# Kernel tuning notes

Measured on AMD Instinct MI355X. Metric: run time of the kernel, lower is better.

Reference implementation:

```python
import jax, jax.numpy as jnp
import numpy as np

B, S, N, F = 4, 256, 128, 64
D = 128          # d_model == 2*F so encoder/decoder dims agree
NH = 4           # hard-coded num_heads in both MHA blocks


def _linear(x, w, b):
    # torch nn.Linear: y = x @ W.T + b, W: (out, in)
    return x @ w.T + b


def _mha(q, k, v, w_in, b_in, w_out, b_out, nh):
    # torch nn.MultiheadAttention (batch_first=True) with packed in_proj
    bq, sq, e = q.shape
    hd = e // nh
    qp = _linear(q, w_in[:e], b_in[:e])
    kp = _linear(k, w_in[e:2 * e], b_in[e:2 * e])
    vp = _linear(v, w_in[2 * e:], b_in[2 * e:])
    qh = qp.reshape(bq, sq, nh, hd)
    kh = kp.reshape(bq, k.shape[1], nh, hd)
    vh = vp.reshape(bq, v.shape[1], nh, hd)
    scores = jnp.einsum('bqhd,bkhd->bhqk', qh, kh) / np.sqrt(hd).astype(np.float32)
    attn = jax.nn.softmax(scores, axis=-1)
    out = jnp.einsum('bhqk,bkhd->bqhd', attn, vh).reshape(bq, sq, e)
    return _linear(out, w_out, b_out)


def _pos_enc(s, d):
    pos = jnp.arange(s, dtype=jnp.float32)[:, None]
    div = jnp.exp(jnp.arange(0, d, 2, dtype=jnp.float32) * (-np.log(10000.0) / d))
    pe = jnp.zeros((s, d), dtype=jnp.float32)
    pe = pe.at[:, 0::2].set(jnp.sin(pos * div))
    pe = pe.at[:, 1::2].set(jnp.cos(pos * div))
    return pe


def _haar_decouple(x):
    # exact vectorized pywt haar dwt + single-branch idwt (even seq_len)
    b, s, n, f = x.shape
    pairs = x.reshape(b, s // 2, 2, n, f)
    avg = (pairs[:, :, 0] + pairs[:, :, 1]) * 0.5  # idwt(cA, None) value
    dif = (pairs[:, :, 0] - pairs[:, :, 1]) * 0.5  # idwt(None, cD) value
    x_l = jnp.stack([avg, avg], axis=2).reshape(b, s, n, f)
    x_h = jnp.stack([dif, -dif], axis=2).reshape(b, s, n, f)
    return x_l, x_h


def setup_inputs() -> dict:
    key = jax.random.key(0)
    ks = jax.random.split(key, 32)
    p = lambda i, shp: jax.random.normal(ks[i], shp, jnp.float32) * 0.02
    return {
        'x': jax.random.normal(ks[0], (B, S, N, F), jnp.float32),
        'ts': jax.random.randint(ks[1], (B, S), 0, 252),
        'ta_w_in': p(2, (3 * D, D)), 'ta_b_in': p(3, (3 * D,)),
        'ta_w_out': p(4, (D, D)), 'ta_b_out': p(5, (D,)),
        'conv_w': p(6, (D, 2 * F, 3)), 'conv_b': p(7, (D,)),
        'pl_w': p(8, (D, D)), 'pl_b': p(9, (D,)),
        'ph_w': p(10, (D, D)), 'ph_b': p(11, (D,)),
        'as_w_in': p(12, (3 * D, D)), 'as_b_in': p(13, (3 * D,)),
        'as_w_out': p(14, (D, D)), 'as_b_out': p(15, (D,)),
        'ac_w_in': p(16, (3 * D, D)), 'ac_b_in': p(17, (3 * D,)),
        'ac_w_out': p(18, (D, D)), 'ac_b_out': p(19, (D,)),
        'rl_w': p(20, (1, D)), 'rl_b': p(21, (1,)),
        'cl_w': p(22, (2, D)), 'cl_b': p(23, (2,)),
        'rf_w': p(24, (1, D)), 'rf_b': p(25, (1,)),
        'cf_w': p(26, (2, D)), 'cf_b': p(27, (2,)),
    }


def reference(x, ts, ta_w_in, ta_b_in, ta_w_out, ta_b_out, conv_w, conv_b,
              pl_w, pl_b, ph_w, ph_b, as_w_in, as_b_in, as_w_out, as_b_out,
              ac_w_in, ac_b_in, ac_w_out, ac_b_out, rl_w, rl_b, cl_w, cl_b,
              rf_w, rf_b, cf_w, cf_b):
    b, s, n, f = x.shape
    # --- DecouplingFlowLayer (vectorized haar) ---
    x_l, x_h = _haar_decouple(x)
    xl_cat = jnp.concatenate([x, x_l], axis=-1)  # (b,s,n,2f)
    xh_cat = jnp.concatenate([x, x_h], axis=-1)
    e = 2 * f
    # --- DualFrequencyEncoder ---
    pe = _pos_enc(s, e)
    xl_flat = xl_cat.transpose(0, 2, 1, 3).reshape(b * n, s, e) + pe
    x_tatt = _mha(xl_flat, xl_flat, xl_flat, ta_w_in, ta_b_in, ta_w_out, ta_b_out, NH)
    x_l_gat = x_tatt.reshape(b, s, n, e)  # faithful raw .view() as in torch
    xh_flat = xh_cat.transpose(0, 2, 3, 1).reshape(b * n, e, s)
    conv = jax.lax.conv_general_dilated(
        xh_flat, conv_w, window_strides=(1,), padding=[(2, 2)],
        rhs_dilation=(2,), dimension_numbers=('NCH', 'OIH', 'NCH'))
    conv = jax.nn.relu(conv + conv_b[None, :, None])
    x_h_gat = conv.reshape(b, n, -1, s).transpose(0, 3, 1, 2)  # (b,s,n,D)
    d = x_h_gat.shape[-1]
    # ts -> time_embedding is computed then discarded in the original forward: dead code
    # --- DualFrequencyFusionDecoder ---
    y_l = x_l_gat.reshape(b * n, s, d)
    y_h = x_h_gat.reshape(b * n, s, d)
    q_l = _linear(y_l, pl_w, pl_b)
    k_h = _linear(y_h, ph_w, ph_b)
    y_l2 = _linear(q_l, pl_w, pl_b)  # predictor_l applied twice, as in torch
    lreg = _linear(y_l2, rl_w, rl_b).reshape(b, s, n)
    lcla = jax.nn.softmax(_linear(y_l2, cl_w, cl_b), axis=-1).reshape(b, s, n, 2)
    a_self = _mha(q_l, q_l, q_l, as_w_in, as_b_in, as_w_out, as_b_out, NH)
    a_cross = _mha(q_l, k_h, k_h, ac_w_in, ac_b_in, ac_w_out, ac_b_out, NH)
    fused = (a_self + a_cross).reshape(b, s, n, d)
    reg = _linear(fused, rf_w, rf_b)[..., 0]
    cla = jax.nn.softmax(_linear(fused, cf_w, cf_b), axis=-1)
    return reg, cla, lreg, lcla
```

## Files before the change

kernel.cpp:

```cpp
#include <hip/hip_runtime.h>
#include <hip/hip_bf16.h>

typedef __attribute__((ext_vector_type(8))) short short8v;
typedef __attribute__((ext_vector_type(4))) short short4v;
typedef __attribute__((ext_vector_type(4))) float f32x4;
typedef __hip_bfloat16 bh;

constexpr long SF_ELEMS = 131072L * 128;
#define MFMA16(a, b, c) __builtin_amdgcn_mfma_f32_16x16x32_bf16((a), (b), (c), 0, 0, 0)

__device__ __forceinline__ short bh_bits(float x) {
  bh h = __float2bfloat16(x);
  return *reinterpret_cast<short*>(&h);
}


__global__ __launch_bounds__(256) void sf_wcvt(const float* __restrict__ s0, const float* __restrict__ s1,
                                               const float* __restrict__ s2, const float* __restrict__ s3,
                                               const float* __restrict__ s4, const float* __restrict__ s5,
                                               const float* __restrict__ s6, const float* __restrict__ s7,
                                               const float* __restrict__ cw,
                                               bh* __restrict__ dst) {
  int i = blockIdx.x * 256 + threadIdx.x;
  float v;
  if      (i <  49152) v = s0[i];
  else if (i <  65536) v = s1[i - 49152];
  else if (i <  81920) v = s2[i - 65536];
  else if (i <  98304) v = s3[i - 81920];
  else if (i < 147456) v = s4[i - 98304];
  else if (i < 163840) v = s5[i - 147456];
  else if (i < 212992) v = s6[i - 163840];
  else if (i < 229376) v = s7[i - 212992];
  else if (i < 278528) {
    int j = i - 229376;
    int tap = j >> 14, rem = j & 16383;
    v = cw[rem * 3 + tap];
  } else if (i < 294912) {
    int j = i - 278528;
    v = s2[(j & 127) * 128 + (j >> 7)];
  } else if (i < 311296) {
    int j = i - 294912;
    v = s3[(j & 127) * 128 + (j >> 7)];
  } else return;
  dst[i] = __float2bfloat16(v);
}

__global__ __launch_bounds__(256) void sf_pe(float* __restrict__ pe) {
  int i = blockIdx.x * 256 + threadIdx.x;
  int e = i & 127, s = i >> 7;
  int ii = e >> 1;
  float dv = expf(-0.0719557945041855f * (float)(2 * ii));
  float ang = (float)s * dv;
  pe[i] = (e & 1) ? cosf(ang) : sinf(ang);
}

__global__ __launch_bounds__(256) void sf_foldw(const bh* __restrict__ A0) {
  __shared__ bh Lw[4][32][140];
  const int t = threadIdx.x, lane = t & 63, w = t >> 6;
  const int lr = lane & 15, lg = lane >> 4;
  const f32x4 z4 = {0.f, 0.f, 0.f, 0.f};
  const bh* Xp; const bh* Bp; bh* Op;
  int blk = blockIdx.x;
  bh* A = const_cast<bh*>(A0);
  if (blk < 3)      { Xp = A0 + 163840 + blk * 16384; Bp = A0 + 278528; Op = A + 311296 + blk * 16384; }
  else if (blk == 3){ Xp = A0 + 98304;                Bp = A0 + 278528; Op = A + 360448; }
  else if (blk == 4){ Xp = A0 + 98304 + 16384;        Bp = A0 + 294912; Op = A + 376832; }
  else if (blk == 5){ Xp = A0 + 98304 + 32768;        Bp = A0 + 294912; Op = A + 393216; }
  else              { Xp = A0 + 65536;                Bp = A0 + 278528; Op = A + 409600; }
  const long R0 = (long)w * 32;
  short8v a[2][4];
#pragma unroll
  for (int ks = 0; ks < 4; ++ks) {
    a[0][ks] = *reinterpret_cast<const short8v*>(Xp + (R0 + lr) * 128 + ks * 32 + lg * 8);
    a[1][ks] = *reinterpret_cast<const short8v*>(Xp + (R0 + 16 + lr) * 128 + ks * 32 + lg * 8);
  }
  f32x4 acc[2][8];
#pragma unroll
  for (int m = 0; m < 2; ++m)
#pragma unroll
    for (int n = 0; n < 8; ++n) acc[m][n] = z4;
#pragma unroll
  for (int ks = 0; ks < 4; ++ks)
#pragma unroll
    for (int n = 0; n < 8; ++n) {
      short8v b = *reinterpret_cast<const short8v*>(Bp + (long)(n * 16 + lr) * 128 + ks * 32 + lg * 8);
      acc[0][n] = MFMA16(a[0][ks], b, acc[0][n]);
      acc[1][n] = MFMA16(a[1][ks], b, acc[1][n]);
    }
#pragma unroll
  for (int n = 0; n < 8; ++n)
#pragma unroll
    for (int m = 0; m < 2; ++m)
#pragma unroll
      for (int r = 0; r < 4; ++r)
        Lw[w][m * 16 + 4 * lg + r][n * 16 + lr] = __float2bfloat16(acc[m][n][r]);
#pragma unroll
  for (int c = 0; c < 8; ++c) {
    int row_l = c * 4 + lg;
    short8v v = *reinterpret_cast<const short8v*>(&Lw[w][row_l][lr * 8]);
    *reinterpret_cast<short8v*>(Op + (R0 + row_l) * 128 + lr * 8) = v;
  }
}

__global__ __launch_bounds__(256) void sf_foldb(const float* __restrict__ as_w, const float* __restrict__ as_b,
                                                const float* __restrict__ ac_w, const float* __restrict__ ac_b,
                                                const float* __restrict__ pl_w, const float* __restrict__ pl_b,
                                                const float* __restrict__ ph_b,
                                                float* __restrict__ FB) {
  int i = blockIdx.x * 256 + threadIdx.x;
  if (i >= 896) return;
  const float* w1; const float* b2; float b1;
  if (i < 384)      { w1 = as_w + (long)i * 128;           b2 = pl_b; b1 = as_b[i]; }
  else if (i < 512) { w1 = ac_w + (long)(i - 384) * 128;   b2 = pl_b; b1 = ac_b[i - 384]; }
  else if (i < 640) { w1 = ac_w + (long)(i - 512 + 128) * 128; b2 = ph_b; b1 = ac_b[i - 512 + 128]; }
  else if (i < 768) { w1 = ac_w + (long)(i - 640 + 256) * 128; b2 = ph_b; b1 = ac_b[i - 640 + 256]; }
  else              { w1 = pl_w + (long)(i - 768) * 128;   b2 = pl_b; b1 = pl_b[i - 768]; }
  float d = b1;
  for (int k = 0; k < 128; ++k) d = fmaf(w1[k], b2[k], d);
  FB[i] = d;
}

__global__ __launch_bounds__(256) void sf_buildzx(const float* __restrict__ x,
                                                  const float* __restrict__ pe,
                                                  bh* __restrict__ z,
                                                  bh* __restrict__ xh) {
  long i = (long)blockIdx.x * 256 + threadIdx.x;
  if (i >= SF_ELEMS) return;
  int e = (int)(i & 127);
  int s = (int)((i >> 7) & 255);
  int r = (int)(i >> 15);
  int b = r >> 7, stk = r & 127;
  float zv, hv;
  if (e < 64) {
    float val = x[(((long)b * 256 + s) * 128 + stk) * 64 + e];
    zv = val; hv = val;
  } else {
    int f = e - 64;
    int t2 = s >> 1;
    float a0 = x[(((long)b * 256 + 2 * t2) * 128 + stk) * 64 + f];
    float a1 = x[(((long)b * 256 + 2 * t2 + 1) * 128 + stk) * 64 + f];
    zv = 0.5f * (a0 + a1);
    float d = 0.5f * (a0 - a1);
    hv = (s & 1) ? -d : d;
  }
  z[i] = __float2bfloat16(zv + pe[s * 128 + e]);
  xh[i] = __float2bfloat16(hv);
}

__global__ __launch_bounds__(256) void sf_attnp(const bh* Qsrc, const bh* KVsrc,
                                                const bh* __restrict__ Win,
                                                const float* __restrict__ bin,
                                                bh* __restrict__ O) {
  __shared__ bh Ks[256][36];
  __shared__ bh Vt[32][260];
  __shared__ bh QP[4][64][36];
  const int t = threadIdx.x, lane = t & 63, w = t >> 6;
  const int lr = lane & 15, lg = lane >> 4;
  const int bn = blockIdx.x >> 2, h = blockIdx.x & 3;
  const long R0 = (long)bn * 256;
  const int ch = h * 32;
  const f32x4 z4 = {0.f, 0.f, 0.f, 0.f};
  const float SC2 = 0.2550351f;
  {
    short8v wq[2][4];
#pragma unroll
    for (int n = 0; n < 2; ++n)
#pragma unroll
      for (int ks = 0; ks < 4; ++ks)
        wq[n][ks] = *reinterpret_cast<const short8v*>(Win + (long)(ch + n * 16 + lr) * 128 + ks * 32 + lg * 8);
#pragma unroll
    for (int m2 = 0; m2 < 4; ++m2) {
      short8v asv[4];
#pragma unroll
      for (int ks = 0; ks < 4; ++ks)
        asv[ks] = *reinterpret_cast<const short8v*>(Qsrc + (R0 + w * 64 + m2 * 16 + lr) * 128 + ks * 32 + lg * 8);
#pragma unroll
      for (int n = 0; n < 2; ++n) {
        f32x4 acc = z4;
#pragma unroll
        for (int ks = 0; ks < 4; ++ks) acc = MFMA16(asv[ks], wq[n][ks], acc);
        float bb = bin[ch + n * 16 + lr];
#pragma unroll
        for (int r = 0; r < 4; ++r)
          QP[w][m2 * 16 + 4 * lg + r][n * 16 + lr] = __float2bfloat16((acc[r] + bb) * SC2);
      }
    }
  }
  {
    short8v wk[2][4], wv[2][4];
#pragma unroll
    for (int n = 0; n < 2; ++n)
#pragma unroll
      for (int ks = 0; ks < 4; ++ks) {
        wk[n][ks] = *reinterpret_cast<const short8v*>(Win + (long)(128 + ch + n * 16 + lr) * 128 + ks * 32 + lg * 8);
        wv[n][ks] = *reinterpret_cast<const short8v*>(Win + (long)(256 + ch + n * 16 + lr) * 128 + ks * 32 + lg * 8);
      }
#pragma unroll
    for (int m2 = 0; m2 < 4; ++m2) {
      short8v asv[4];
#pragma unroll
      for (int ks = 0; ks < 4; ++ks)
        asv[ks] = *reinterpret_cast<const short8v*>(KVsrc + (R0 + w * 64 + m2 * 16 + lr) * 128 + ks * 32 + lg * 8);
#pragma unroll
      for (int n = 0; n < 2; ++n) {
        f32x4 ak = z4, av = z4;
#pragma unroll
        for (int ks = 0; ks < 4; ++ks) {
          ak = MFMA16(asv[ks], wk[n][ks], ak);
          av = MFMA16(asv[ks], wv[n][ks], av);
        }
        float bk = bin[128 + ch + n * 16 + lr];
        float bv = bin[256 + ch + n * 16 + lr];
#pragma unroll
        for (int r = 0; r < 4; ++r)
          Ks[w * 64 + m2 * 16 + 4 * lg + r][n * 16 + lr] = __float2bfloat16(ak[r] + bk);
        short4v pv;
#pragma unroll
        for (int r = 0; r < 4; ++r) pv[r] = bh_bits(av[r] + bv);
        *reinterpret_cast<short4v*>(&Vt[n * 16 + lr][w * 64 + m2 * 16 + 4 * lg]) = pv;
      }
    }
  }
  __syncthreads();
  short8v aq[4];
#pragma unroll
  for (int mt = 0; mt < 4; ++mt)
    aq[mt] = *reinterpret_cast<const short8v*>(&QP[w][mt * 16 + lr][lg * 8]);
  bh* plp = &QP[w][0][0];
  f32x4 Oacc[4][2];
  float psum[4] = {0.f, 0.f, 0.f, 0.f};
#pragma unroll
  for (int mt = 0; mt < 4; ++mt) { Oacc[mt][0] = z4; Oacc[mt][1] = z4; }
#pragma unroll
  for (int kt = 0; kt < 4; ++kt) {
    short8v bvf[2][2];
#pragma unroll
    for (int dt = 0; dt < 2; ++dt)
#pragma unroll
      for (int ks = 0; ks < 2; ++ks)
        bvf[dt][ks] = *reinterpret_cast<const short8v*>(&Vt[dt * 16 + lr][kt * 64 + ks * 32 + lg * 8]);
#pragma unroll
    for (int mt = 0; mt < 4; ++mt) {
      f32x4 st[4];
#pragma unroll
      for (int nt = 0; nt < 4; ++nt) {
        short8v bk = *reinterpret_cast<const short8v*>(&Ks[kt * 64 + nt * 16 + lr][lg * 8]);
        st[nt] = MFMA16(bk, aq[mt], z4);
      }
      float ps = 0.f;
#pragma unroll
      for (int nt = 0; nt < 4; ++nt) {
        float p0 = exp2f(st[nt][0]);
        float p1 = exp2f(st[nt][1]);
        float p2 = exp2f(st[nt][2]);
        float p3 = exp2f(st[nt][3]);
        ps += (p0 + p1) + (p2 + p3);
        short4v pk;
        pk[0] = bh_bits(p0); pk[1] = bh_bits(p1); pk[2] = bh_bits(p2); pk[3] = bh_bits(p3);
        *reinterpret_cast<short4v*>(&plp[lr * 72 + nt * 16 + 4 * lg]) = pk;
      }
      psum[mt] += ps;
#pragma unroll
      for (int ks = 0; ks < 2; ++ks) {
        short8v ap = *reinterpret_cast<const short8v*>(&plp[lr * 72 + ks * 32 + lg * 8]);
        Oacc[mt][0] = MFMA16(ap, bvf[0][ks], Oacc[mt][0]);
        Oacc[mt][1] = MFMA16(ap, bvf[1][ks], Oacc[mt][1]);
      }
    }
  }
#pragma unroll
  for (int mt = 0; mt < 4; ++mt) {
    float ps = psum[mt];
    ps += __shfl_xor(ps, 16, 64);
    ps += __shfl_xor(ps, 32, 64);
    float inv = 1.f / ps;
#pragma unroll
    for (int r = 0; r < 4; ++r) {
      float invr = __shfl(inv, 4 * lg + r, 64);
      long row = R0 + w * 64 + mt * 16 + 4 * lg + r;
      O[row * 128 + ch + lr]      = __float2bfloat16(Oacc[mt][0][r] * invr);
      O[row * 128 + ch + 16 + lr] = __float2bfloat16(Oacc[mt][1][r] * invr);
    }
  }
}

__global__ __launch_bounds__(256) void sf_convy(const bh* __restrict__ Xh,
                                                const bh* __restrict__ Wr,
                                                const float* __restrict__ cbias,
                                                bh* __restrict__ Yh) {
  __shared__ bh Lw[4][32][140];
  const int t = threadIdx.x, lane = t & 63, w = t >> 6;
  const int lr = lane & 15, lg = lane >> 4;
  const int bnc = blockIdx.x >> 1;
  const int half = blockIdx.x & 1;
  const int b = bnc >> 7, stk = bnc & 127;
  const int R0 = half * 128 + w * 32;
  const f32x4 z4 = {0.f, 0.f, 0.f, 0.f};
  const short8v zf = {0, 0, 0, 0, 0, 0, 0, 0};
  f32x4 acc[2][8];
#pragma unroll
  for (int m = 0; m < 2; ++m)
#pragma unroll
    for (int n = 0; n < 8; ++n) acc[m][n] = z4;
#pragma unroll
  for (int tap = 0; tap < 3; ++tap) {
    const int shift = 2 * tap - 2;
#pragma unroll
    for (int ks = 0; ks < 4; ++ks) {
      int s0 = R0 + lr + shift;
      int s1 = s0 + 16;
      short8v a0 = zf, a1 = zf;
      if ((unsigned)s0 < 256u)
        a0 = *reinterpret_cast<const short8v*>(Xh + ((long)bnc * 256 + s0) * 128 + ks * 32 + lg * 8);
      if ((unsigned)s1 < 256u)
        a1 = *reinterpret_cast<const short8v*>(Xh + ((long)bnc * 256 + s1) * 128 + ks * 32 + lg * 8);
#pragma unroll
      for (int n = 0; n < 8; ++n) {
        short8v bb = *reinterpret_cast<const short8v*>(Wr + (long)tap * 16384 + (long)(n * 16 + lr) * 128 + ks * 32 + lg * 8);
        acc[0][n] = MFMA16(a0, bb, acc[0][n]);
        acc[1][n] = MFMA16(a1, bb, acc[1][n]);
      }
    }
  }
#pragma unroll
  for (int n = 0; n < 8; ++n) {
    float bv = cbias[n * 16 + lr];
#pragma unroll
    for (int m = 0; m < 2; ++m)
#pragma unroll
      for (int r = 0; r < 4; ++r)
        Lw[w][m * 16 + 4 * lg + r][n * 16 + lr] = __float2bfloat16(fmaxf(acc[m][n][r] + bv, 0.f));
  }
#pragma unroll
  for (int c = 0; c < 8; ++c) {
    int row_l = c * 4 + lg;
    int sc = R0 + row_l;
    int rp = b * 128 + (sc >> 1);
    int sp = ((sc & 1) << 7) + stk;
    short8v v = *reinterpret_cast<const short8v*>(&Lw[w][row_l][lr * 8]);
    *reinterpret_cast<short8v*>(Yh + ((long)rp * 256 + sp) * 128 + lr * 8) = v;
  }
}

__global__ __launch_bounds__(256) void sf_encdec(const bh* __restrict__ X,
                                                 const bh* __restrict__ Wo, const float* __restrict__ bo,
                                                 const bh* __restrict__ Wpl2, const float* __restrict__ bpl2,
                                                 const float* __restrict__ rw, const float* __restrict__ rb,
                                                 const float* __restrict__ cw, const float* __restrict__ cb,
                                                 bh* __restrict__ Yl, float* __restrict__ out,
                                                 long off_reg, long off_cla) {
  __shared__ bh Lw[4][32][140];
  __shared__ float hw[3][128];
  const int t = threadIdx.x, lane = t & 63, w = t >> 6;
  const int lr = lane & 15, lg = lane >> 4;
  const long R0 = (long)blockIdx.x * 128 + w * 32;
  const f32x4 z4 = {0.f, 0.f, 0.f, 0.f};
  if (t < 128) { hw[0][t] = rw[t]; hw[1][t] = cw[t]; hw[2][t] = cw[128 + t]; }
  {
    short8v a[2][4];
#pragma unroll
    for (int ks = 0; ks < 4; ++ks) {
      a[0][ks] = *reinterpret_cast<const short8v*>(X + (R0 + lr) * 128 + ks * 32 + lg * 8);
      a[1][ks] = *reinterpret_cast<const short8v*>(X + (R0 + 16 + lr) * 128 + ks * 32 + lg * 8);
    }
    f32x4 acc[2][8];
#pragma unroll
    for (int m = 0; m < 2; ++m)
#pragma unroll
      for (int n = 0; n < 8; ++n) acc[m][n] = z4;
#pragma unroll
    for (int ks = 0; ks < 4; ++ks)
#pragma unroll
      for (int n = 0; n < 8; ++n) {
        short8v b = *reinterpret_cast<const short8v*>(Wo + (long)(n * 16 + lr) * 128 + ks * 32 + lg * 8);
        acc[0][n] = MFMA16(a[0][ks], b, acc[0][n]);
        acc[1][n] = MFMA16(a[1][ks], b, acc[1][n]);
      }
#pragma unroll
    for (int n = 0; n < 8; ++n) {
      float bv = bo[n * 16 + lr];
#pragma unroll
      for (int m = 0; m < 2; ++m)
#pragma unroll
        for (int r = 0; r < 4; ++r)
          Lw[w][m * 16 + 4 * lg + r][n * 16 + lr] = __float2bfloat16(acc[m][n][r] + bv);
    }
#pragma unroll
    for (int c = 0; c < 8; ++c) {
      int row_l = c * 4 + lg;
      short8v v = *reinterpret_cast<const short8v*>(&Lw[w][row_l][lr * 8]);
      *reinterpret_cast<short8v*>(Yl + (R0 + row_l) * 128 + lr * 8) = v;
    }
  }
  {
    short8v a[2][4];
#pragma unroll
    for (int ks = 0; ks < 4; ++ks) {
      a[0][ks] = *reinterpret_cast<const short8v*>(&Lw[w][lr][ks * 32 + lg * 8]);
      a[1][ks] = *reinterpret_cast<const short8v*>(&Lw[w][16 + lr][ks * 32 + lg * 8]);
    }
    f32x4 acc[2][8];
#pragma unroll
    for (int m = 0; m < 2; ++m)
#pragma unroll
      for (int n = 0; n < 8; ++n) acc[m][n] = z4;
#pragma unroll
    for (int ks = 0; ks < 4; ++ks)
#pragma unroll
      for (int n = 0; n < 8; ++n) {
        short8v b = *reinterpret_cast<const short8v*>(Wpl2 + (long)(n * 16 + lr) * 128 + ks * 32 + lg * 8);
        acc[0][n] = MFMA16(a[0][ks], b, acc[0][n]);
        acc[1][n] = MFMA16(a[1][ks], b, acc[1][n]);
      }
#pragma unroll
    for (int n = 0; n < 8; ++n) {
      float bv = bpl2[n * 16 + lr];
#pragma unroll
      for (int m = 0; m < 2; ++m)
#pragma unroll
        for (int r = 0; r < 4; ++r)
          Lw[w][m * 16 + 4 * lg + r][n * 16 + lr] = __float2bfloat16(acc[m][n][r] + bv);
    }
  }
  __syncthreads();
  {
    const int rr = lane >> 1, hh = lane & 1;
    float d0 = 0.f, d1 = 0.f, d2 = 0.f;
#pragma unroll
    for (int j = 0; j < 8; ++j) {
      short8v v8 = *reinterpret_cast<const short8v*>(&Lw[w][rr][hh * 64 + j * 8]);
      const bh* vv = reinterpret_cast<const bh*>(&v8);
#pragma unroll
      for (int k = 0; k < 8; ++k) {
        float f = __bfloat162float(vv[k]);
        int c = hh * 64 + j * 8 + k;
        d0 = fmaf(f, hw[0][c], d0);
        d1 = fmaf(f, hw[1][c], d1);
        d2 = fmaf(f, hw[2][c], d2);
      }
    }
    d0 += __shfl_xor(d0, 1, 64);
    d1 += __shfl_xor(d1, 1, 64);
    d2 += __shfl_xor(d2, 1, 64);
    if (hh == 0) {
      long row = R0 + rr;
      d0 += rb[0]; d1 += cb[0]; d2 += cb[1];
      float mx = fmaxf(d1, d2);
      float e1 = __expf(d1 - mx), e2 = __expf(d2 - mx);
      float inv = 1.f / (e1 + e2);
      out[off_reg + row] = d0;
      out[off_cla + row * 2] = e1 * inv;
      out[off_cla + row * 2 + 1] = e2 * inv;
    }
  }
}

__global__ __launch_bounds__(256) void sf_fin2(const bh* __restrict__ Xs,
                                               const bh* __restrict__ Was, const float* __restrict__ bs,
                                               const bh* __restrict__ Xc,
                                               const bh* __restrict__ Wac, const float* __restrict__ bc,
                                               const float* __restrict__ rw, const float* __restrict__ rb,
                                               const float* __restrict__ cw, const float* __restrict__ cb,
                                               float* __restrict__ out, long off_reg, long off_cla) {
  __shared__ bh Lw[4][32][140];
  __shared__ float hw[3][128];
  const int t = threadIdx.x, lane = t & 63, w = t >> 6;
  const int lr = lane & 15, lg = lane >> 4;
  const long R0 = (long)blockIdx.x * 128 + w * 32;
  const f32x4 z4 = {0.f, 0.f, 0.f, 0.f};
  if (t < 128) { hw[0][t] = rw[t]; hw[1][t] = cw[t]; hw[2][t] = cw[128 + t]; }
  {
    f32x4 acc[2][8];
#pragma unroll
    for (int m = 0; m < 2; ++m)
#pragma unroll
      for (int n = 0; n < 8; ++n) acc[m][n] = z4;
    {
      short8v a[2][4];
#pragma unroll
      for (int ks = 0; ks < 4; ++ks) {
        a[0][ks] = *reinterpret_cast<const short8v*>(Xs + (R0 + lr) * 128 + ks * 32 + lg * 8);
        a[1][ks] = *reinterpret_cast<const short8v*>(Xs + (R0 + 16 + lr) * 128 + ks * 32 + lg * 8);
      }
#pragma unroll
      for (int ks = 0; ks < 4; ++ks)
#pragma unroll
        for (int n = 0; n < 8; ++n) {
          short8v b = *reinterpret_cast<const short8v*>(Was + (long)(n * 16 + lr) * 128 + ks * 32 + lg * 8);
          acc[0][n] = MFMA16(a[0][ks], b, acc[0][n]);
          acc[1][n] = MFMA16(a[1][ks], b, acc[1][n]);
        }
    }
    {
      short8v a[2][4];
#pragma unroll
      for (int ks = 0; ks < 4; ++ks) {
        a[0][ks] = *reinterpret_cast<const short8v*>(Xc + (R0 + lr) * 128 + ks * 32 + lg * 8);
        a[1][ks] = *reinterpret_cast<const short8v*>(Xc + (R0 + 16 + lr) * 128 + ks * 32 + lg * 8);
      }
#pragma unroll
      for (int ks = 0; ks < 4; ++ks)
#pragma unroll
        for (int n = 0; n < 8; ++n) {
          short8v b = *reinterpret_cast<const short8v*>(Wac + (long)(n * 16 + lr) * 128 + ks * 32 + lg * 8);
          acc[0][n] = MFMA16(a[0][ks], b, acc[0][n]);
          acc[1][n] = MFMA16(a[1][ks], b, acc[1][n]);
        }
    }
#pragma unroll
    for (int n = 0; n < 8; ++n) {
      float bv = bs[n * 16 + lr] + bc[n * 16 + lr];
#pragma unroll
      for (int m = 0; m < 2; ++m)
#pragma unroll
        for (int r = 0; r < 4; ++r)
          Lw[w][m * 16 + 4 * lg + r][n * 16 + lr] = __float2bfloat16(acc[m][n][r] + bv);
    }
  }
  __syncthreads();
  {
    const int rr = lane >> 1, hh = lane & 1;
    float d0 = 0.f, d1 = 0.f, d2 = 0.f;
#pragma unroll
    for (int j = 0; j < 8; ++j) {
      short8v v8 = *reinterpret_cast<const short8v*>(&Lw[w][rr][hh * 64 + j * 8]);
      const bh* vv = reinterpret_cast<const bh*>(&v8);
#pragma unroll
      for (int k = 0; k < 8; ++k) {
        float f = __bfloat162float(vv[k]);
        int c = hh * 64 + j * 8 + k;
        d0 = fmaf(f, hw[0][c], d0);
        d1 = fmaf(f, hw[1][c], d1);
        d2 = fmaf(f, hw[2][c], d2);
      }
    }
    d0 += __shfl_xor(d0, 1, 64);
    d1 += __shfl_xor(d1, 1, 64);
    d2 += __shfl_xor(d2, 1, 64);
    if (hh == 0) {
      long row = R0 + rr;
      d0 += rb[0]; d1 += cb[0]; d2 += cb[1];
      float mx = fmaxf(d1, d2);
      float e1 = __expf(d1 - mx), e2 = __expf(d2 - mx);
      float inv = 1.f / (e1 + e2);
      out[off_reg + row] = d0;
      out[off_cla + row * 2] = e1 * inv;
      out[off_cla + row * 2 + 1] = e2 * inv;
    }
  }
}

extern "C" void kernel_launch(void* const* d_in, const int* in_sizes, int n_in,
                              void* d_out, int out_size, void* d_ws, size_t ws_size,
                              hipStream_t stream) {
  (void)in_sizes; (void)n_in; (void)out_size; (void)ws_size;
  const float* x       = (const float*)d_in[0];
  const float* ta_w_in = (const float*)d_in[2];
  const float* ta_b_in = (const float*)d_in[3];
  const float* ta_w_o  = (const float*)d_in[4];
  const float* ta_b_o  = (const float*)d_in[5];
  const float* conv_w  = (const float*)d_in[6];
  const float* conv_b  = (const float*)d_in[7];
  const float* pl_w    = (const float*)d_in[8];
  const float* pl_b    = (const float*)d_in[9];
  const float* ph_w    = (const float*)d_in[10];
  const float* ph_b    = (const float*)d_in[11];
  const float* as_w_in = (const float*)d_in[12];
  const float* as_b_in = (const float*)d_in[13];
  const float* as_w_o  = (const float*)d_in[14];
  const float* as_b_o  = (const float*)d_in[15];
  const float* ac_w_in = (const float*)d_in[16];
  const float* ac_b_in = (const float*)d_in[17];
  const float* ac_w_o  = (const float*)d_in[18];
  const float* ac_b_o  = (const float*)d_in[19];
  const float* rl_w    = (const float*)d_in[20];
  const float* rl_b    = (const float*)d_in[21];
  const float* cl_w    = (const float*)d_in[22];
  const float* cl_b    = (const float*)d_in[23];
  const float* rf_w    = (const float*)d_in[24];
  const float* rf_b    = (const float*)d_in[25];
  const float* cf_w    = (const float*)d_in[26];
  const float* cf_b    = (const float*)d_in[27];
  float* out = (float*)d_out;

  bh* S0 = (bh*)d_ws;
  bh* S1 = S0 + SF_ELEMS;
  bh* S2 = S1 + SF_ELEMS;
  bh* S3 = S2 + SF_ELEMS;
  bh* S4 = S3 + SF_ELEMS;
  bh* A  = S4 + SF_ELEMS;
  float* PE = (float*)(A + 425984);
  float* FB = PE + 32768;

  dim3 blk(256);
  const int GZ = (int)(SF_ELEMS / 256);
  const int GL = 1024;

  sf_wcvt<<<1216, blk, 0, stream>>>(ta_w_in, ta_w_o, pl_w, ph_w, ac_w_in, ac_w_o,
                                    as_w_in, as_w_o, conv_w, A);
  sf_pe<<<128, blk, 0, stream>>>(PE);
  sf_foldb<<<4, blk, 0, stream>>>(as_w_in, as_b_in, ac_w_in, ac_b_in,
                                  pl_w, pl_b, ph_b, FB);
  sf_foldw<<<7, blk, 0, stream>>>(A);

  sf_buildzx<<<GZ, blk, 0, stream>>>(x, PE, S0, S3);
  sf_attnp<<<2048, blk, 0, stream>>>(S0, S0, A, ta_b_in, S1);
  sf_encdec<<<GL, blk, 0, stream>>>(S1, A + 49152, ta_b_o, A + 409600, FB + 768,
                                    rl_w, rl_b, cl_w, cl_b, S2, out,
                                    393216L, 524288L);
  sf_convy<<<1024, blk, 0, stream>>>(S3, A + 229376, conv_b, S4);

  sf_attnp<<<2048, blk, 0, stream>>>(S2, S4, A + 360448, FB + 384, S3);

  sf_attnp<<<2048, blk, 0, stream>>>(S2, S2, A + 311296, FB, S1);

  sf_fin2<<<GL, blk, 0, stream>>>(S1, A + 212992, as_b_o, S3, A + 147456, ac_b_o,
                                  rf_w, rf_b, cf_w, cf_b, out, 0L, 131072L);
}
```

Measured before the change: 451.7 us.

## Keep softmax probabilities in registers via ds_bpermute instead of LDS round-trip

The attention kernel no longer writes exp'd probabilities to a shared-memory scratch and reads them back. It packs them into bf16 pairs and redistributes them across lanes with ds_bpermute, then swaps the MFMA operand order so the output is produced transposed. It also drops the QP shared buffer by staging Q through Ks scratch, uses the hardware exp2 builtin, and writes outputs as 4-wide vector stores without shuffles. This lowers LDS footprint and traffic, and may raise occupancy. The cost is extra permute instructions and lane-select logic.

```diff
diff --git a/kernel.cpp b/kernel.cpp
--- a/kernel.cpp
+++ b/kernel.cpp
@@ -8,10 +8,15 @@
 
 constexpr long SF_ELEMS = 131072L * 128;
 #define MFMA16(a, b, c) __builtin_amdgcn_mfma_f32_16x16x32_bf16((a), (b), (c), 0, 0, 0)
+#define EXP2F(x) __builtin_amdgcn_exp2f(x)
 
 __device__ __forceinline__ short bh_bits(float x) {
   bh h = __float2bfloat16(x);
   return *reinterpret_cast<short*>(&h);
+}
+__device__ __forceinline__ int pack2bh(float a, float b) {
+  return (int)(((unsigned)(unsigned short)bh_bits(a)) |
+               (((unsigned)(unsigned short)bh_bits(b)) << 16));
 }
 
 
@@ -153,7 +158,6 @@
                                                 bh* __restrict__ O) {
   __shared__ bh Ks[256][36];
   __shared__ bh Vt[32][260];
-  __shared__ bh QP[4][64][36];
   const int t = threadIdx.x, lane = t & 63, w = t >> 6;
   const int lr = lane & 15, lg = lane >> 4;
   const int bn = blockIdx.x >> 2, h = blockIdx.x & 3;
@@ -161,7 +165,9 @@
   const int ch = h * 32;
   const f32x4 z4 = {0.f, 0.f, 0.f, 0.f};
   const float SC2 = 0.2550351f;
+  short8v aq[4];
   {
+    bh* scr = &Ks[w * 64][0];
     short8v wq[2][4];
 #pragma unroll
     for (int n = 0; n < 2; ++n)
@@ -182,8 +188,9 @@
         float bb = bin[ch + n * 16 + lr];
 #pragma unroll
         for (int r = 0; r < 4; ++r)
-          QP[w][m2 * 16 + 4 * lg + r][n * 16 + lr] = __float2bfloat16((acc[r] + bb) * SC2);
-      }
+          scr[(4 * lg + r) * 36 + n * 16 + lr] = __float2bfloat16((acc[r] + bb) * SC2);
+      }
+      aq[m2] = *reinterpret_cast<const short8v*>(&scr[lr * 36 + lg * 8]);
     }
   }
   {
@@ -222,11 +229,9 @@
     }
   }
   __syncthreads();
-  short8v aq[4];
-#pragma unroll
-  for (int mt = 0; mt < 4; ++mt)
-    aq[mt] = *reinterpret_cast<const short8v*>(&QP[w][mt * 16 + lr][lg * 8]);
-  bh* plp = &QP[w][0][0];
+  const int addrA = ((2 * (lg & 1)) * 16 + lr) * 4;
+  const int addrB = addrA + 64;
+  const bool hiHalf = (lg >= 2);
   f32x4 Oacc[4][2];
   float psum[4] = {0.f, 0.f, 0.f, 0.f};
 #pragma unroll
@@ -247,24 +252,31 @@
         short8v bk = *reinterpret_cast<const short8v*>(&Ks[kt * 64 + nt * 16 + lr][lg * 8]);
         st[nt] = MFMA16(bk, aq[mt], z4);
       }
+      int pk2[4][2];
       float ps = 0.f;
 #pragma unroll
       for (int nt = 0; nt < 4; ++nt) {
-        float p0 = exp2f(st[nt][0]);
-        float p1 = exp2f(st[nt][1]);
-        float p2 = exp2f(st[nt][2]);
-        float p3 = exp2f(st[nt][3]);
+        float p0 = EXP2F(st[nt][0]);
+        float p1 = EXP2F(st[nt][1]);
+        float p2 = EXP2F(st[nt][2]);
+        float p3 = EXP2F(st[nt][3]);
         ps += (p0 + p1) + (p2 + p3);
-        short4v pk;
-        pk[0] = bh_bits(p0); pk[1] = bh_bits(p1); pk[2] = bh_bits(p2); pk[3] = bh_bits(p3);
-        *reinterpret_cast<short4v*>(&plp[lr * 72 + nt * 16 + 4 * lg]) = pk;
+        pk2[nt][0] = pack2bh(p0, p1);
+        pk2[nt][1] = pack2bh(p2, p3);
       }
       psum[mt] += ps;
 #pragma unroll
       for (int ks = 0; ks < 2; ++ks) {
-        short8v ap = *reinterpret_cast<const short8v*>(&plp[lr * 72 + ks * 32 + lg * 8]);
-        Oacc[mt][0] = MFMA16(ap, bvf[0][ks], Oacc[mt][0]);
-        Oacc[mt][1] = MFMA16(ap, bvf[1][ks], Oacc[mt][1]);
+        union { int i[4]; short8v v; } pf;
+#pragma unroll
+        for (int j = 0; j < 4; ++j) {
+          int ad = (j < 2) ? addrA : addrB;
+          int lo = __builtin_amdgcn_ds_bpermute(ad, pk2[2 * ks][j & 1]);
+          int hi = __builtin_amdgcn_ds_bpermute(ad, pk2[2 * ks + 1][j & 1]);
+          pf.i[j] = hiHalf ? hi : lo;
+        }
+        Oacc[mt][0] = MFMA16(bvf[0][ks], pf.v, Oacc[mt][0]);
+        Oacc[mt][1] = MFMA16(bvf[1][ks], pf.v, Oacc[mt][1]);
       }
     }
   }
@@ -274,12 +286,13 @@
     ps += __shfl_xor(ps, 16, 64);
     ps += __shfl_xor(ps, 32, 64);
     float inv = 1.f / ps;
-#pragma unroll
-    for (int r = 0; r < 4; ++r) {
-      float invr = __shfl(inv, 4 * lg + r, 64);
-      long row = R0 + w * 64 + mt * 16 + 4 * lg + r;
-      O[row * 128 + ch + lr]      = __float2bfloat16(Oacc[mt][0][r] * invr);
-      O[row * 128 + ch + 16 + lr] = __float2bfloat16(Oacc[mt][1][r] * invr);
+    long row = R0 + w * 64 + mt * 16 + lr;
+#pragma unroll
+    for (int dt = 0; dt < 2; ++dt) {
+      short4v ov;
+#pragma unroll
+      for (int r = 0; r < 4; ++r) ov[r] = bh_bits(Oacc[mt][dt][r] * inv);
+      *reinterpret_cast<short4v*>(O + row * 128 + ch + dt * 16 + 4 * lg) = ov;
     }
   }
 }
```

Result: no change. 458.8 us (+1.6%).

## Fuse self-attention and dilated conv into one heterogeneous launch

Applied to the files above, without the earlier changes.

Moves the attention and convolution kernel bodies into device functions that share one pooled shared-memory buffer. A new combined kernel interleaves conv blocks with self-attention blocks (one conv per two attention blocks), so the two independent stages run concurrently in a single 3072-block launch, and the separate self-attention launch is dropped. The aim is to fill the GPU better and remove a launch plus its tail. The cost is that conv blocks now get the larger attention-sized LDS allocation, which can lower their occupancy, and the blocks have uneven run times.

```diff
diff --git a/kernel.cpp b/kernel.cpp
--- a/kernel.cpp
+++ b/kernel.cpp
@@ -147,16 +147,16 @@
   xh[i] = __float2bfloat16(hv);
 }
 
-__global__ __launch_bounds__(256) void sf_attnp(const bh* Qsrc, const bh* KVsrc,
-                                                const bh* __restrict__ Win,
-                                                const float* __restrict__ bin,
-                                                bh* __restrict__ O) {
-  __shared__ bh Ks[256][36];
-  __shared__ bh Vt[32][260];
-  __shared__ bh QP[4][64][36];
+__device__ __forceinline__ void attn_core(const bh* Qsrc, const bh* KVsrc,
+                                          const bh* __restrict__ Win,
+                                          const float* __restrict__ bin,
+                                          bh* __restrict__ O, int bn, int h,
+                                          bh* pool) {
+  bh (*Ks)[36] = reinterpret_cast<bh(*)[36]>(pool);
+  bh (*Vt)[260] = reinterpret_cast<bh(*)[260]>(pool + 9216);
+  bh (*QP)[64][36] = reinterpret_cast<bh(*)[64][36]>(pool + 17536);
   const int t = threadIdx.x, lane = t & 63, w = t >> 6;
   const int lr = lane & 15, lg = lane >> 4;
-  const int bn = blockIdx.x >> 2, h = blockIdx.x & 3;
   const long R0 = (long)bn * 256;
   const int ch = h * 32;
   const f32x4 z4 = {0.f, 0.f, 0.f, 0.f};
@@ -284,15 +284,16 @@
   }
 }
 
-__global__ __launch_bounds__(256) void sf_convy(const bh* __restrict__ Xh,
-                                                const bh* __restrict__ Wr,
-                                                const float* __restrict__ cbias,
-                                                bh* __restrict__ Yh) {
-  __shared__ bh Lw[4][32][140];
+__device__ __forceinline__ void conv_core(const bh* __restrict__ Xh,
+                                          const bh* __restrict__ Wr,
+                                          const float* __restrict__ cbias,
+                                          bh* __restrict__ Yh, int bid,
+                                          bh* pool) {
+  bh (*Lw)[32][140] = reinterpret_cast<bh(*)[32][140]>(pool);
   const int t = threadIdx.x, lane = t & 63, w = t >> 6;
   const int lr = lane & 15, lg = lane >> 4;
-  const int bnc = blockIdx.x >> 1;
-  const int half = blockIdx.x & 1;
+  const int bnc = bid >> 1;
+  const int half = bid & 1;
   const int b = bnc >> 7, stk = bnc & 127;
   const int R0 = half * 128 + w * 32;
   const f32x4 z4 = {0.f, 0.f, 0.f, 0.f};
@@ -339,6 +340,33 @@
     int sp = ((sc & 1) << 7) + stk;
     short8v v = *reinterpret_cast<const short8v*>(&Lw[w][row_l][lr * 8]);
     *reinterpret_cast<short8v*>(Yh + ((long)rp * 256 + sp) * 128 + lr * 8) = v;
+  }
+}
+
+__global__ __launch_bounds__(256) void sf_attnp(const bh* Qsrc, const bh* KVsrc,
+                                                const bh* __restrict__ Win,
+                                                const float* __restrict__ bin,
+                                                bh* __restrict__ O) {
+  __shared__ bh pool[26880];
+  attn_core(Qsrc, KVsrc, Win, bin, O, blockIdx.x >> 2, blockIdx.x & 3, pool);
+}
+
+__global__ __launch_bounds__(256) void sf_selfconv(const bh* Q,
+                                                   const bh* __restrict__ Win,
+                                                   const float* __restrict__ bin,
+                                                   bh* __restrict__ Os,
+                                                   const bh* __restrict__ Xh,
+                                                   const bh* __restrict__ Wr,
+                                                   const float* __restrict__ cbias,
+                                                   bh* __restrict__ Yh) {
+  __shared__ bh pool[26880];
+  int g = blockIdx.x;
+  int m3 = g % 3, q3 = g / 3;
+  if (m3 == 2) {
+    conv_core(Xh, Wr, cbias, Yh, q3, pool);
+  } else {
+    int aid = q3 * 2 + m3;
+    attn_core(Q, Q, Win, bin, Os, aid >> 2, aid & 3, pool);
   }
 }
 
@@ -608,11 +636,11 @@
   sf_encdec<<<GL, blk, 0, stream>>>(S1, A + 49152, ta_b_o, A + 409600, FB + 768,
                                     rl_w, rl_b, cl_w, cl_b, S2, out,
                                     393216L, 524288L);
-  sf_convy<<<1024, blk, 0, stream>>>(S3, A + 229376, conv_b, S4);
+
+  sf_selfconv<<<3072, blk, 0, stream>>>(S2, A + 311296, FB, S1,
+                                        S3, A + 229376, conv_b, S4);
 
   sf_attnp<<<2048, blk, 0, stream>>>(S2, S4, A + 360448, FB + 384, S3);
-
-  sf_attnp<<<2048, blk, 0, stream>>>(S2, S2, A + 311296, FB, S1);
 
   sf_fin2<<<GL, blk, 0, stream>>>(S1, A + 212992, as_b_o, S3, A + 147456, ac_b_o,
                                   rf_w, rf_b, cf_w, cf_b, out, 0L, 131072L);
```

New measurement: 480.3 us. 1.06x slower.
